# Performance work log

Hardware: AMD Instinct MI355X
Metric: run time of the kernel (lower is better)

The kernel has to match this reference:

```python
import jax, jax.numpy as jnp
import numpy as np

MARGIN = 0.2
LAMBDA_SOFTMAX = 9.0
LAMBDA_LSE = 6.0
WEIGHT_FACTOR = 0.7  # attn_prev is absent/zero on the i2t path
EPS = 1e-8
NEG_INF = -1e9


def setup_inputs() -> dict:
    key = jax.random.key(0)
    k1, k2, k3 = jax.random.split(key, 3)
    B, R, W, D = 128, 36, 32, 256  # batch, regions, max words, feat dim
    im = jax.random.normal(k1, (B, R, D), jnp.float32)
    s = jax.random.normal(k2, (B, W, D), jnp.float32)
    s_l = jax.random.randint(k3, (B,), 1, W + 1)  # caption lengths in [1, W]
    return {"im": im, "s": s, "s_l": s_l}


def _xattn_scores_i2t(im, s, s_l):
    # im: (B, R, D) images; s: (C, W, D) captions; s_l: (C,) lengths
    C, W = s.shape[0], s.shape[1]
    word_mask = jnp.arange(W)[None, :] < s_l[:, None]  # (C, W)

    # func_attention(query=images, context=caption words):
    # attn[c,b,w,r] = <s[c,w], im[b,r]>
    attn = jnp.einsum('cwd,brd->cbwr', s, im)
    # raw_feature_norm == 'clipped_l2norm': LeakyReLU(0.1) then l2norm over region axis
    attn = jax.nn.leaky_relu(attn, 0.1)
    attn = attn / (jnp.sqrt(jnp.sum(attn * attn, axis=-1, keepdims=True)) + EPS)
    # softmax over sourceL = words, with smoothing; mask padded words
    logits = jnp.where(word_mask[:, None, :, None], attn * LAMBDA_SOFTMAX, NEG_INF)
    A = jax.nn.softmax(logits, axis=2)  # (C, B, W, R), sums to 1 over words
    # weightedContext[c,b,r,:] = 0.7 * sum_w A[c,b,w,r] * s[c,w,:]
    wC = WEIGHT_FACTOR * jnp.einsum('cbwr,cwd->cbrd', A, s)

    # cosine similarity between image regions and weighted caption context
    num = jnp.sum(im[None] * wC, axis=-1)                      # (C, B, R)
    denom = jnp.linalg.norm(im, axis=-1)[None] * jnp.linalg.norm(wC, axis=-1)
    row_sim = num / jnp.clip(denom, EPS)

    # agg_func == 'LogSumExp' over regions
    sim = jax.nn.logsumexp(LAMBDA_LSE * row_sim, axis=2) / LAMBDA_LSE  # (C, B)
    return sim.T  # scores: (n_image, n_caption)


def reference(im, s, s_l):
    scores = _xattn_scores_i2t(im, s, s_l)
    diag = jnp.diag(scores)
    cost_s = jnp.clip(MARGIN + scores - diag[:, None], 0.0)   # caption retrieval
    cost_im = jnp.clip(MARGIN + scores - diag[None, :], 0.0)  # image retrieval
    eye = jnp.eye(scores.shape[0], dtype=bool)
    cost_s = jnp.where(eye, 0.0, cost_s)
    cost_im = jnp.where(eye, 0.0, cost_im)
    # max_violation=True: hardest negatives
    return jnp.sum(jnp.max(cost_s, axis=1)) + jnp.sum(jnp.max(cost_im, axis=0))
```

## Files before the change

### kernel.cpp

```cpp
#include <hip/hip_runtime.h>
#include <math.h>

#define CN 128
#define RN 36
#define WN 32
#define DN 256

#define SSTR  264
#define GSTR  40
#define ATSTR 40

#define WS_SCORES 0
#define WS_S_SW   65536
#define WS_IM_SW  (WS_S_SW + CN*16384)
#define WS_N2I    (WS_IM_SW + CN*18432)
#define WS_NEED   (WS_N2I + CN*RN*4)

typedef unsigned short u16;
typedef __attribute__((ext_vector_type(4))) unsigned short u16x4;
typedef __attribute__((ext_vector_type(8))) unsigned short u16x8;
typedef __attribute__((ext_vector_type(8))) __bf16 bf16x8;
typedef __attribute__((ext_vector_type(4))) float f32x4;

#define C9   12.9842502f
#define C6   8.65616798f
#define IC6  0.115524530f

__device__ __forceinline__ float bf2f(u16 u){ return __uint_as_float(((unsigned)u)<<16); }
__device__ __forceinline__ u16 f2bf(float f){ unsigned x=__float_as_uint(f); return (u16)((x + 0x7fffu + ((x>>16)&1u))>>16); }
__device__ __forceinline__ u16 f2bf_hw(float f){ __bf16 h = (__bf16)f; return __builtin_bit_cast(u16, h); }
__device__ __forceinline__ float lrelu(float v){ return fmaxf(v, 0.1f*v); }

__device__ __forceinline__ void gload16(const void* g, void* l){
    __builtin_amdgcn_global_load_lds((const __attribute__((address_space(1))) void*)g,
                                     (__attribute__((address_space(3))) void*)l, 16, 0, 0);
}

__global__ __launch_bounds__(256)
void precompute_kernel(const float* __restrict__ im, const float* __restrict__ s,
                       char* __restrict__ ws)
{
    const int tid = threadIdx.x;
    if (blockIdx.x < 128) {
        const int i = blockIdx.x;
        const float* src = s + (size_t)i*(WN*DN);
#pragma unroll
        for (int it = 0; it < 4; it++) {
            int idx = tid + it*256;
            int h = idx >> 9, r = (idx >> 4) & 31, x = idx & 15;
            int jl = x ^ (r & 7);
            const float4* p = (const float4*)(src + r*DN + h*128 + jl*8);
            float4 v0 = p[0], v1 = p[1];
            u16x8 hh = { f2bf(v0.x),f2bf(v0.y),f2bf(v0.z),f2bf(v0.w),
                         f2bf(v1.x),f2bf(v1.y),f2bf(v1.z),f2bf(v1.w) };
            *(u16x8*)(ws + WS_S_SW + (size_t)h*1048576 + (size_t)i*8192 + r*256 + x*16) = hh;
        }
    } else {
        const int i = blockIdx.x - 128;
        const float* src = im + (size_t)i*(RN*DN);
#pragma unroll
        for (int it = 0; it < 5; it++) {
            int idx = tid + it*256;
            if (idx < 1152) {
                int q = idx / 288, rem = idx - q*288;
                int r = rem >> 3, x = rem & 7;
                int jl = x ^ (r & 7);
                const float4* p = (const float4*)(src + r*DN + q*64 + jl*8);
                float4 v0 = p[0], v1 = p[1];
                u16x8 hh = { f2bf(v0.x),f2bf(v0.y),f2bf(v0.z),f2bf(v0.w),
                             f2bf(v1.x),f2bf(v1.y),f2bf(v1.z),f2bf(v1.w) };
                *(u16x8*)(ws + WS_IM_SW + (size_t)q*589824 + (size_t)i*4608 + r*128 + x*16) = hh;
            }
        }
        float* n2o = (float*)(ws + WS_N2I) + (size_t)i*RN;
#pragma unroll
        for (int it = 0; it < 2; it++) {
            int idx = tid + it*256;
            if (idx < 288) {
                int r = idx >> 3, q = idx & 7;
                const float4* p = (const float4*)(src + r*DN + q*32);
                float ss = 0.f;
#pragma unroll
                for (int k = 0; k < 8; k++) {
                    float4 v = p[k];
                    ss = fmaf(v.x,v.x,ss); ss = fmaf(v.y,v.y,ss);
                    ss = fmaf(v.z,v.z,ss); ss = fmaf(v.w,v.w,ss);
                }
                ss += __shfl_xor(ss,1); ss += __shfl_xor(ss,2); ss += __shfl_xor(ss,4);
                if (q == 0) n2o[r] = ss;
            }
        }
    }
}

__global__ __launch_bounds__(512, 4)
void xattn_staged(const int* __restrict__ s_l, char* __restrict__ ws)
{
    __shared__ __align__(16) u16 smem[19968];
    u16* lds_s  = smem;
    u16* lds_im = smem + 8192;
    u16* lds_g  = smem + 17408;
    char* sB = (char*)smem;

    const int tid = threadIdx.x;
    const int lane = tid & 63, wv = tid >> 6;
    const int bq = blockIdx.x, cp = blockIdx.y;
    const int ci = wv >> 2, bi = wv & 3;
    const int c = cp*2 + ci, b = bq*4 + bi;
    const int col = lane & 15, g4 = lane >> 4;
    const int gm = bi >> 1, gn = bi & 1;
    const int L = s_l[c];
    const int r2c = (32+col > 35) ? 35 : 32+col;

    const char* im_base = ws + WS_IM_SW + (size_t)(bq*4)*4608;
    const char* s_base  = ws + WS_S_SW  + (size_t)(cp*2)*8192;

    auto stageq = [&](int q){
        const int tot = (q & 1) ? 18 : 34;
        const char* imsrc = im_base + (size_t)q*589824;
        const char* ssrc  = s_base  + (size_t)(q>>1)*1048576;
#pragma unroll
        for (int t = 0; t < 5; t++) {
            int blk = wv + t*8;
            if (blk < tot) {
                const char* src; char* dst;
                if (blk < 18) { src = imsrc + blk*1024;      dst = sB + 16384 + blk*1024; }
                else          { src = ssrc + (blk-18)*1024;  dst = sB + (blk-18)*1024; }
                gload16(src + lane*16, dst);
            }
        }
    };

    const float* n2p = (const float*)(ws + WS_N2I) + (size_t)b*RN;
    float n2v0 = n2p[col];
    float n2v1 = n2p[16+col];
    float n2v2 = n2p[r2c];

    f32x4 raw[2][3];
#pragma unroll
    for (int m = 0; m < 2; m++)
#pragma unroll
        for (int n = 0; n < 3; n++) raw[m][n] = (f32x4){0.f,0.f,0.f,0.f};
    f32x4 gacc = {0.f,0.f,0.f,0.f};

    const u16* sbb = lds_s + ci*4096;
    const u16* ibb = lds_im + bi*2304;

    auto computeq = [&](int q){
#pragma unroll
        for (int ks = 0; ks < 2; ks++) {
            int chS = (q&1)*8 + ks*4 + g4;
            int chI = ks*4 + g4;
            int oA  = (chS ^ (col&7)) * 8;
            int oB  = (chI ^ (col&7)) * 8;
            int oB2 = (chI ^ (r2c&7)) * 8;
            bf16x8 a0 = *(const bf16x8*)&sbb[col*128 + oA];
            bf16x8 a1 = *(const bf16x8*)&sbb[(16+col)*128 + oA];
            bf16x8 b0 = *(const bf16x8*)&ibb[col*64 + oB];
            bf16x8 b1 = *(const bf16x8*)&ibb[(16+col)*64 + oB];
            bf16x8 b2 = *(const bf16x8*)&ibb[r2c*64 + oB2];
            bf16x8 ga = *(const bf16x8*)&sbb[(gm*16+col)*128 + oA];
            bf16x8 gb = *(const bf16x8*)&sbb[(gn*16+col)*128 + oA];
            raw[0][0] = __builtin_amdgcn_mfma_f32_16x16x32_bf16(a0, b0, raw[0][0], 0,0,0);
            raw[0][1] = __builtin_amdgcn_mfma_f32_16x16x32_bf16(a0, b1, raw[0][1], 0,0,0);
            raw[0][2] = __builtin_amdgcn_mfma_f32_16x16x32_bf16(a0, b2, raw[0][2], 0,0,0);
            raw[1][0] = __builtin_amdgcn_mfma_f32_16x16x32_bf16(a1, b0, raw[1][0], 0,0,0);
            raw[1][1] = __builtin_amdgcn_mfma_f32_16x16x32_bf16(a1, b1, raw[1][1], 0,0,0);
            raw[1][2] = __builtin_amdgcn_mfma_f32_16x16x32_bf16(a1, b2, raw[1][2], 0,0,0);
            gacc      = __builtin_amdgcn_mfma_f32_16x16x32_bf16(ga, gb, gacc, 0,0,0);
        }
    };

    stageq(0); __syncthreads();
    computeq(0); __syncthreads();
    stageq(1); __syncthreads();
    computeq(1); __syncthreads();
    stageq(2); __syncthreads();
    computeq(2); __syncthreads();
    stageq(3); __syncthreads();
    computeq(3);

    {
        u16x4 hg = { f2bf_hw(gacc[0]), f2bf_hw(gacc[1]), f2bf_hw(gacc[2]), f2bf_hw(gacc[3]) };
        *(u16x4*)&lds_g[ci*1280 + (gn*16+col)*GSTR + gm*16 + g4*4] = hg;
    }

    float af[2][3][4];
#pragma unroll
    for (int m = 0; m < 2; m++) {
#pragma unroll
        for (int reg = 0; reg < 4; reg++) {
            float ssum = 0.f;
#pragma unroll
            for (int n = 0; n < 3; n++) {
                float v = lrelu(raw[m][n][reg]);
                if (n == 2 && col >= 4) v = 0.f;
                af[m][n][reg] = v;
                ssum = fmaf(v, v, ssum);
            }
            ssum += __shfl_xor(ssum, 1);
            ssum += __shfl_xor(ssum, 2);
            ssum += __shfl_xor(ssum, 4);
            ssum += __shfl_xor(ssum, 8);
            float inv2 = C9 / (sqrtf(ssum) + 1e-8f);
#pragma unroll
            for (int n = 0; n < 3; n++) af[m][n][reg] *= inv2;
        }
    }

    float num[3];
#pragma unroll
    for (int n = 0; n < 3; n++) {
        float nm = 0.f;
#pragma unroll
        for (int m = 0; m < 2; m++)
#pragma unroll
            for (int reg = 0; reg < 4; reg++) {
                int w = m*16 + g4*4 + reg;
                float e = (w < L) ? __builtin_amdgcn_exp2f(af[m][n][reg]) : 0.f;
                af[m][n][reg] = e;
                nm = fmaf(e, raw[m][n][reg], nm);
            }
        nm += __shfl_xor(nm, 16);
        nm += __shfl_xor(nm, 32);
        num[n] = nm;
    }

    __syncthreads();

    u16* at = smem + wv*1920;
#pragma unroll
    for (int m = 0; m < 2; m++)
#pragma unroll
        for (int n = 0; n < 3; n++) {
            u16x4 h = { f2bf_hw(af[m][n][0]), f2bf_hw(af[m][n][1]),
                        f2bf_hw(af[m][n][2]), f2bf_hw(af[m][n][3]) };
            *(u16x4*)&at[(n*16 + col)*ATSTR + m*16 + g4*4] = h;
        }

    bf16x8 gf0 = *(const bf16x8*)&lds_g[ci*1280 + col*GSTR + g4*8];
    bf16x8 gf1 = *(const bf16x8*)&lds_g[ci*1280 + (16+col)*GSTR + g4*8];

    float qv[3];
#pragma unroll
    for (int n = 0; n < 3; n++) {
        bf16x8 bfv = *(const bf16x8*)&at[(n*16 + col)*ATSTR + g4*8];
        f32x4 z = {0.f,0.f,0.f,0.f};
        f32x4 t0 = __builtin_amdgcn_mfma_f32_16x16x32_bf16(gf0, bfv, z, 0,0,0);
        f32x4 t1 = __builtin_amdgcn_mfma_f32_16x16x32_bf16(gf1, bfv, z, 0,0,0);
        float q = 0.f;
#pragma unroll
        for (int reg = 0; reg < 4; reg++) {
            q = fmaf(af[0][n][reg], t0[reg], q);
            q = fmaf(af[1][n][reg], t1[reg], q);
        }
        q += __shfl_xor(q, 16);
        q += __shfl_xor(q, 32);
        qv[n] = q;
    }

    float rs[3];
    {
        float n2a[3] = { n2v0, n2v1, n2v2 };
#pragma unroll
        for (int n = 0; n < 3; n++) {
            float denom = fmaxf(0.7f * sqrtf(n2a[n] * qv[n]), 1e-8f);
            rs[n] = 0.7f * num[n] / denom;
        }
    }
    float xm = -1e30f;
#pragma unroll
    for (int n = 0; n < 3; n++) {
        bool valid = (n < 2) || (col < 4);
        if (valid) xm = fmaxf(xm, C6 * rs[n]);
    }
    xm = fmaxf(xm, __shfl_xor(xm, 1));
    xm = fmaxf(xm, __shfl_xor(xm, 2));
    xm = fmaxf(xm, __shfl_xor(xm, 4));
    xm = fmaxf(xm, __shfl_xor(xm, 8));
    float es = 0.f;
#pragma unroll
    for (int n = 0; n < 3; n++) {
        bool valid = (n < 2) || (col < 4);
        if (valid) es += __builtin_amdgcn_exp2f(C6 * rs[n] - xm);
    }
    es += __shfl_xor(es, 1);
    es += __shfl_xor(es, 2);
    es += __shfl_xor(es, 4);
    es += __shfl_xor(es, 8);

    if (lane == 0)
        ((float*)(ws + WS_SCORES))[(size_t)b * CN + c] =
            (xm + __builtin_amdgcn_logf(es)) * IC6;
}

__global__ __launch_bounds__(512, 2)
void xattn_fallback(const float* __restrict__ im, const float* __restrict__ s,
                    const int* __restrict__ s_l, float* __restrict__ scores)
{
    __shared__ u16   s_lds[2][WN*SSTR];
    __shared__ u16   im_lds[4][RN*SSTR];
    __shared__ u16   g_lds[2][WN*GSTR];
    __shared__ u16   at_lds[8][48*ATSTR];
    __shared__ float n2i_lds[4][RN];

    const int tid  = threadIdx.x;
    const int lane = tid & 63;
    const int wv   = tid >> 6;
    const int bq   = blockIdx.x, cp = blockIdx.y;
    const int ci   = wv >> 2, bi = wv & 3;
    const int c    = cp*2 + ci, b = bq*4 + bi;
    const int col  = lane & 15, g4 = lane >> 4;

    if (wv < 4) {
        const float4* g = (const float4*)(im + (size_t)(bq*4 + wv) * (RN*DN));
        u16* dst = im_lds[wv];
#pragma unroll
        for (int k = 0; k < 36; k++) {
            int i = lane + k*64;
            float4 v = g[i];
            int row = i >> 6, cc = (i & 63) * 4;
            u16x4 h = { f2bf(v.x), f2bf(v.y), f2bf(v.z), f2bf(v.w) };
            *(u16x4*)&dst[row*SSTR + cc] = h;
        }
    } else {
        int cap = (wv - 4) >> 1;
        int l2  = ((wv - 4) & 1) * 64 + lane;
        const float4* g = (const float4*)(s + (size_t)(cp*2 + cap) * (WN*DN));
        u16* dst = s_lds[cap];
#pragma unroll
        for (int k = 0; k < 16; k++) {
            int i = l2 + k*128;
            float4 v = g[i];
            int row = i >> 6, cc = (i & 63) * 4;
            u16x4 h = { f2bf(v.x), f2bf(v.y), f2bf(v.z), f2bf(v.w) };
            *(u16x4*)&dst[row*SSTR + cc] = h;
        }
    }
    __syncthreads();

    {
        const int gm = (wv >> 1) & 1, gn = wv & 1;
        const u16* sb = s_lds[ci];
        f32x4 acc = {0.f, 0.f, 0.f, 0.f};
#pragma unroll
        for (int ks = 0; ks < 8; ks++) {
            int k0 = ks*32 + g4*8;
            bf16x8 af = *(const bf16x8*)&sb[(gm*16 + col)*SSTR + k0];
            bf16x8 bfv = *(const bf16x8*)&sb[(gn*16 + col)*SSTR + k0];
            acc = __builtin_amdgcn_mfma_f32_16x16x32_bf16(af, bfv, acc, 0, 0, 0);
        }
        u16x4 h = { f2bf(acc[0]), f2bf(acc[1]), f2bf(acc[2]), f2bf(acc[3]) };
        *(u16x4*)&g_lds[ci][(gn*16 + col)*GSTR + gm*16 + g4*4] = h;
    }

    if (wv < 4) {
        const u16* ib = im_lds[wv];
        int r = lane >> 1, half = lane & 1;
        float ss = 0.f;
        const u16x8* p = (const u16x8*)&ib[r*SSTR + half*128];
#pragma unroll
        for (int k = 0; k < 16; k++) {
            u16x8 v = p[k];
#pragma unroll
            for (int j = 0; j < 8; j++) { float f = bf2f(v[j]); ss = fmaf(f, f, ss); }
        }
        ss += __shfl_xor(ss, 1);
        if (half == 0) n2i_lds[wv][r] = ss;
        if (lane < 8) {
            int r2 = 32 + (lane >> 1), h2 = lane & 1;
            float s2 = 0.f;
            const u16x8* p2 = (const u16x8*)&ib[r2*SSTR + h2*128];
#pragma unroll
            for (int k = 0; k < 16; k++) {
                u16x8 v = p2[k];
#pragma unroll
                for (int j = 0; j < 8; j++) { float f = bf2f(v[j]); s2 = fmaf(f, f, s2); }
            }
            s2 += __shfl_xor(s2, 1);
            if (h2 == 0) n2i_lds[wv][r2] = s2;
        }
    }

    const u16* sb = s_lds[ci];
    const u16* ib = im_lds[bi];
    f32x4 raw[2][3];
#pragma unroll
    for (int m = 0; m < 2; m++)
#pragma unroll
        for (int n = 0; n < 3; n++) raw[m][n] = (f32x4){0.f,0.f,0.f,0.f};
    {
        int r2c = 32 + col; if (r2c > 35) r2c = 35;
#pragma unroll
        for (int ks = 0; ks < 8; ks++) {
            int k0 = ks*32 + g4*8;
            bf16x8 a0 = *(const bf16x8*)&sb[col*SSTR + k0];
            bf16x8 a1 = *(const bf16x8*)&sb[(16 + col)*SSTR + k0];
            bf16x8 b0 = *(const bf16x8*)&ib[col*SSTR + k0];
            bf16x8 b1 = *(const bf16x8*)&ib[(16 + col)*SSTR + k0];
            bf16x8 b2 = *(const bf16x8*)&ib[r2c*SSTR + k0];
            raw[0][0] = __builtin_amdgcn_mfma_f32_16x16x32_bf16(a0, b0, raw[0][0], 0,0,0);
            raw[0][1] = __builtin_amdgcn_mfma_f32_16x16x32_bf16(a0, b1, raw[0][1], 0,0,0);
            raw[0][2] = __builtin_amdgcn_mfma_f32_16x16x32_bf16(a0, b2, raw[0][2], 0,0,0);
            raw[1][0] = __builtin_amdgcn_mfma_f32_16x16x32_bf16(a1, b0, raw[1][0], 0,0,0);
            raw[1][1] = __builtin_amdgcn_mfma_f32_16x16x32_bf16(a1, b1, raw[1][1], 0,0,0);
            raw[1][2] = __builtin_amdgcn_mfma_f32_16x16x32_bf16(a1, b2, raw[1][2], 0,0,0);
        }
    }

    float af[2][3][4];
#pragma unroll
    for (int m = 0; m < 2; m++) {
#pragma unroll
        for (int reg = 0; reg < 4; reg++) {
            float ssum = 0.f;
#pragma unroll
            for (int n = 0; n < 3; n++) {
                float v = lrelu(raw[m][n][reg]);
                if (n == 2 && col >= 4) v = 0.f;
                af[m][n][reg] = v;
                ssum = fmaf(v, v, ssum);
            }
            ssum += __shfl_xor(ssum, 1);
            ssum += __shfl_xor(ssum, 2);
            ssum += __shfl_xor(ssum, 4);
            ssum += __shfl_xor(ssum, 8);
            float inv = 1.0f / (sqrtf(ssum) + 1e-8f);
#pragma unroll
            for (int n = 0; n < 3; n++) af[m][n][reg] *= inv;
        }
    }

    const int L = s_l[c];
    float num[3], qv[3];
#pragma unroll
    for (int n = 0; n < 3; n++) {
        float mx = -1e30f;
#pragma unroll
        for (int m = 0; m < 2; m++)
#pragma unroll
            for (int reg = 0; reg < 4; reg++) {
                int w = m*16 + g4*4 + reg;
                if (w < L) mx = fmaxf(mx, af[m][n][reg]);
            }
        mx = fmaxf(mx, __shfl_xor(mx, 16));
        mx = fmaxf(mx, __shfl_xor(mx, 32));
        mx *= 9.0f;
        float sme = 0.f;
#pragma unroll
        for (int m = 0; m < 2; m++)
#pragma unroll
            for (int reg = 0; reg < 4; reg++) {
                int w = m*16 + g4*4 + reg;
                float e = (w < L) ? __expf(fmaf(9.0f, af[m][n][reg], -mx)) : 0.f;
                af[m][n][reg] = e;
                sme += e;
            }
        sme += __shfl_xor(sme, 16);
        sme += __shfl_xor(sme, 32);
        float inv = 1.0f / sme;
        float nm = 0.f;
#pragma unroll
        for (int m = 0; m < 2; m++)
#pragma unroll
            for (int reg = 0; reg < 4; reg++) {
                af[m][n][reg] *= inv;
                nm = fmaf(af[m][n][reg], raw[m][n][reg], nm);
            }
        nm += __shfl_xor(nm, 16);
        nm += __shfl_xor(nm, 32);
        num[n] = nm;
    }

#pragma unroll
    for (int m = 0; m < 2; m++)
#pragma unroll
        for (int n = 0; n < 3; n++) {
            u16x4 h = { f2bf(af[m][n][0]), f2bf(af[m][n][1]),
                        f2bf(af[m][n][2]), f2bf(af[m][n][3]) };
            *(u16x4*)&at_lds[wv][(n*16 + col)*ATSTR + m*16 + g4*4] = h;
        }

    __syncthreads();

    bf16x8 gf0 = *(const bf16x8*)&g_lds[ci][col*GSTR + g4*8];
    bf16x8 gf1 = *(const bf16x8*)&g_lds[ci][(16+col)*GSTR + g4*8];
    f32x4 tt[2][3];
#pragma unroll
    for (int n = 0; n < 3; n++) {
        bf16x8 bfv = *(const bf16x8*)&at_lds[wv][(n*16 + col)*ATSTR + g4*8];
        f32x4 z = {0.f,0.f,0.f,0.f};
        tt[0][n] = __builtin_amdgcn_mfma_f32_16x16x32_bf16(gf0, bfv, z, 0,0,0);
        tt[1][n] = __builtin_amdgcn_mfma_f32_16x16x32_bf16(gf1, bfv, z, 0,0,0);
    }

#pragma unroll
    for (int n = 0; n < 3; n++) {
        float q = 0.f;
#pragma unroll
        for (int m = 0; m < 2; m++)
#pragma unroll
            for (int reg = 0; reg < 4; reg++) q = fmaf(af[m][n][reg], tt[m][n][reg], q);
        q += __shfl_xor(q, 16);
        q += __shfl_xor(q, 32);
        qv[n] = q;
    }

    float rs[3];
#pragma unroll
    for (int n = 0; n < 3; n++) {
        int r = n*16 + col; if (r > 35) r = 35;
        float n2 = n2i_lds[bi][r];
        float denom = fmaxf(0.7f * sqrtf(n2 * qv[n]), 1e-8f);
        rs[n] = 0.7f * num[n] / denom;
    }
    float xm = -1e30f;
#pragma unroll
    for (int n = 0; n < 3; n++) {
        bool valid = (n < 2) || (col < 4);
        if (valid) xm = fmaxf(xm, 6.0f * rs[n]);
    }
    xm = fmaxf(xm, __shfl_xor(xm, 1));
    xm = fmaxf(xm, __shfl_xor(xm, 2));
    xm = fmaxf(xm, __shfl_xor(xm, 4));
    xm = fmaxf(xm, __shfl_xor(xm, 8));
    float es = 0.f;
#pragma unroll
    for (int n = 0; n < 3; n++) {
        bool valid = (n < 2) || (col < 4);
        if (valid) es += __expf(6.0f * rs[n] - xm);
    }
    es += __shfl_xor(es, 1);
    es += __shfl_xor(es, 2);
    es += __shfl_xor(es, 4);
    es += __shfl_xor(es, 8);

    if (lane == 0) scores[(size_t)b * CN + c] = (xm + __logf(es)) / 6.0f;
}

__global__ __launch_bounds__(1024)
void contrastive_loss_kernel(const float* __restrict__ scores,
                             unsigned int* __restrict__ out)
{
    __shared__ float sc[128][129];
    __shared__ float dg[128];
    __shared__ float red[128];
    const int tid = threadIdx.x;

    const float4* s4 = (const float4*)scores;
#pragma unroll
    for (int it = 0; it < 4; it++) {
        int i = tid + it*1024;
        float4 v = s4[i];
        int row = i >> 5, c4 = (i & 31) << 2;
        sc[row][c4+0] = v.x; sc[row][c4+1] = v.y;
        sc[row][c4+2] = v.z; sc[row][c4+3] = v.w;
    }
    __syncthreads();
    if (tid < 128) dg[tid] = sc[tid][tid];
    __syncthreads();

    const int i = tid >> 3, g = tid & 7;
    const float di = dg[i];
    float rm = 0.f, cm = 0.f;
#pragma unroll
    for (int k = 0; k < 16; k++) {
        int j = g*16 + k;
        if (j != i) {
            rm = fmaxf(rm, 0.2f + sc[i][j] - di);
            cm = fmaxf(cm, 0.2f + sc[j][i] - di);
        }
    }
    rm = fmaxf(rm, __shfl_xor(rm, 1)); cm = fmaxf(cm, __shfl_xor(cm, 1));
    rm = fmaxf(rm, __shfl_xor(rm, 2)); cm = fmaxf(cm, __shfl_xor(cm, 2));
    rm = fmaxf(rm, __shfl_xor(rm, 4)); cm = fmaxf(cm, __shfl_xor(cm, 4));
    if (g == 0) red[i] = rm + cm;
    __syncthreads();

    if (tid < 64) {
        float v = red[tid] + red[tid + 64];
#pragma unroll
        for (int off = 32; off >= 1; off >>= 1) v += __shfl_xor(v, off);
        if (tid == 0) {
            unsigned int x = __float_as_uint(v);
            unsigned int h = (x + 0x7fffu + ((x >> 16) & 1u)) >> 16;
            out[0] = (h << 16) | h;
        }
    }
}

extern "C" void kernel_launch(void* const* d_in, const int* in_sizes, int n_in,
                              void* d_out, int out_size, void* d_ws, size_t ws_size,
                              hipStream_t stream) {
    const float* im  = (const float*)d_in[0];
    const float* s   = (const float*)d_in[1];
    const int*   s_l = (const int*)d_in[2];
    char* ws = (char*)d_ws;

    dim3 grid(32, 64);
    if (ws_size >= (size_t)WS_NEED) {
        precompute_kernel<<<256, 256, 0, stream>>>(im, s, ws);
        xattn_staged<<<grid, 512, 0, stream>>>(s_l, ws);
    } else {
        xattn_fallback<<<grid, 512, 0, stream>>>(im, s, s_l, (float*)ws);
    }
    contrastive_loss_kernel<<<1, 1024, 0, stream>>>((const float*)ws, (unsigned int*)d_out);
}
```

Before: 51.87 us.

## Stage full caption tile once and double-buffer image chunks in LDS

The caption workspace layout changes from split halves to a contiguous per-caption tile. The main kernel now loads the whole caption tile into LDS once and double-buffers the image quarter-chunks, so each compute step overlaps the load of the next chunk and fewer barriers are needed. LDS use roughly doubles and launch bounds drop to 2 blocks per CU, which lowers occupancy. The precompute kernel also switches to hardware bf16 conversion.

```diff
diff --git a/kernel.cpp b/kernel.cpp
--- a/kernel.cpp
+++ b/kernel.cpp
@@ -44,16 +44,17 @@
     if (blockIdx.x < 128) {
         const int i = blockIdx.x;
         const float* src = s + (size_t)i*(WN*DN);
+        u16* out = (u16*)(ws + WS_S_SW) + (size_t)i*8192;
 #pragma unroll
         for (int it = 0; it < 4; it++) {
             int idx = tid + it*256;
-            int h = idx >> 9, r = (idx >> 4) & 31, x = idx & 15;
-            int jl = x ^ (r & 7);
-            const float4* p = (const float4*)(src + r*DN + h*128 + jl*8);
+            int r = idx >> 5, x = idx & 31;
+            int jl = (x & 24) | ((x & 7) ^ (r & 7));
+            const float4* p = (const float4*)(src + r*DN + jl*8);
             float4 v0 = p[0], v1 = p[1];
-            u16x8 hh = { f2bf(v0.x),f2bf(v0.y),f2bf(v0.z),f2bf(v0.w),
-                         f2bf(v1.x),f2bf(v1.y),f2bf(v1.z),f2bf(v1.w) };
-            *(u16x8*)(ws + WS_S_SW + (size_t)h*1048576 + (size_t)i*8192 + r*256 + x*16) = hh;
+            u16x8 hh = { f2bf_hw(v0.x),f2bf_hw(v0.y),f2bf_hw(v0.z),f2bf_hw(v0.w),
+                         f2bf_hw(v1.x),f2bf_hw(v1.y),f2bf_hw(v1.z),f2bf_hw(v1.w) };
+            *(u16x8*)(out + r*256 + x*8) = hh;
         }
     } else {
         const int i = blockIdx.x - 128;
@@ -67,8 +68,8 @@
                 int jl = x ^ (r & 7);
                 const float4* p = (const float4*)(src + r*DN + q*64 + jl*8);
                 float4 v0 = p[0], v1 = p[1];
-                u16x8 hh = { f2bf(v0.x),f2bf(v0.y),f2bf(v0.z),f2bf(v0.w),
-                             f2bf(v1.x),f2bf(v1.y),f2bf(v1.z),f2bf(v1.w) };
+                u16x8 hh = { f2bf_hw(v0.x),f2bf_hw(v0.y),f2bf_hw(v0.z),f2bf_hw(v0.w),
+                             f2bf_hw(v1.x),f2bf_hw(v1.y),f2bf_hw(v1.z),f2bf_hw(v1.w) };
                 *(u16x8*)(ws + WS_IM_SW + (size_t)q*589824 + (size_t)i*4608 + r*128 + x*16) = hh;
             }
         }
@@ -93,14 +94,14 @@
     }
 }
 
-__global__ __launch_bounds__(512, 4)
+__global__ __launch_bounds__(512, 2)
 void xattn_staged(const int* __restrict__ s_l, char* __restrict__ ws)
 {
-    __shared__ __align__(16) u16 smem[19968];
+    __shared__ __align__(16) u16 smem[37376];
     u16* lds_s  = smem;
-    u16* lds_im = smem + 8192;
-    u16* lds_g  = smem + 17408;
-    char* sB = (char*)smem;
+    u16* lds_im = smem + 16384;
+    u16* lds_g  = smem + 34816;
+    char* smem_b = (char*)smem;
 
     const int tid = threadIdx.x;
     const int lane = tid & 63, wv = tid >> 6;
@@ -112,24 +113,29 @@
     const int L = s_l[c];
     const int r2c = (32+col > 35) ? 35 : 32+col;
 
-    const char* im_base = ws + WS_IM_SW + (size_t)(bq*4)*4608;
-    const char* s_base  = ws + WS_S_SW  + (size_t)(cp*2)*8192;
-
-    auto stageq = [&](int q){
-        const int tot = (q & 1) ? 18 : 34;
-        const char* imsrc = im_base + (size_t)q*589824;
-        const char* ssrc  = s_base  + (size_t)(q>>1)*1048576;
-#pragma unroll
-        for (int t = 0; t < 5; t++) {
+    const char* ssrc = ws + WS_S_SW + (size_t)(cp*2)*16384;
+    const char* ibase = ws + WS_IM_SW + (size_t)(bq*4)*4608;
+
+    auto stage_im = [&](int q, int buf){
+        const char* isrc = ibase + (size_t)q*589824;
+        char* dbase = smem_b + 32768 + buf*18432;
+#pragma unroll
+        for (int t = 0; t < 3; t++) {
             int blk = wv + t*8;
-            if (blk < tot) {
-                const char* src; char* dst;
-                if (blk < 18) { src = imsrc + blk*1024;      dst = sB + 16384 + blk*1024; }
-                else          { src = ssrc + (blk-18)*1024;  dst = sB + (blk-18)*1024; }
-                gload16(src + lane*16, dst);
-            }
+            if (blk < 18) gload16(isrc + blk*1024 + lane*16, dbase + blk*1024);
         }
     };
+
+#pragma unroll
+    for (int t = 0; t < 7; t++) {
+        int blk = wv + t*8;
+        if (blk < 50) {
+            const char* src; char* dst;
+            if (blk < 32) { src = ssrc + blk*1024;         dst = smem_b + blk*1024; }
+            else          { src = ibase + (blk-32)*1024;   dst = smem_b + 32768 + (blk-32)*1024; }
+            gload16(src + lane*16, dst);
+        }
+    }
 
     const float* n2p = (const float*)(ws + WS_N2I) + (size_t)b*RN;
     float n2v0 = n2p[col];
@@ -143,24 +149,24 @@
         for (int n = 0; n < 3; n++) raw[m][n] = (f32x4){0.f,0.f,0.f,0.f};
     f32x4 gacc = {0.f,0.f,0.f,0.f};
 
-    const u16* sbb = lds_s + ci*4096;
-    const u16* ibb = lds_im + bi*2304;
-
-    auto computeq = [&](int q){
+    const u16* sbb = lds_s + ci*8192;
+
+    auto computeq = [&](int q, int buf){
+        const u16* ibb = lds_im + buf*9216 + bi*2304;
 #pragma unroll
         for (int ks = 0; ks < 2; ks++) {
-            int chS = (q&1)*8 + ks*4 + g4;
-            int chI = ks*4 + g4;
-            int oA  = (chS ^ (col&7)) * 8;
-            int oB  = (chI ^ (col&7)) * 8;
-            int oB2 = (chI ^ (r2c&7)) * 8;
-            bf16x8 a0 = *(const bf16x8*)&sbb[col*128 + oA];
-            bf16x8 a1 = *(const bf16x8*)&sbb[(16+col)*128 + oA];
+            int chq = ks*4 + g4;
+            int swA = chq ^ (col & 7);
+            int oA  = (q*8 + swA) * 8;
+            int oB  = swA * 8;
+            int oB2 = (chq ^ (r2c & 7)) * 8;
+            bf16x8 a0 = *(const bf16x8*)&sbb[col*256 + oA];
+            bf16x8 a1 = *(const bf16x8*)&sbb[(16+col)*256 + oA];
+            bf16x8 ga = *(const bf16x8*)&sbb[(gm*16+col)*256 + oA];
+            bf16x8 gb = *(const bf16x8*)&sbb[(gn*16+col)*256 + oA];
             bf16x8 b0 = *(const bf16x8*)&ibb[col*64 + oB];
             bf16x8 b1 = *(const bf16x8*)&ibb[(16+col)*64 + oB];
             bf16x8 b2 = *(const bf16x8*)&ibb[r2c*64 + oB2];
-            bf16x8 ga = *(const bf16x8*)&sbb[(gm*16+col)*128 + oA];
-            bf16x8 gb = *(const bf16x8*)&sbb[(gn*16+col)*128 + oA];
             raw[0][0] = __builtin_amdgcn_mfma_f32_16x16x32_bf16(a0, b0, raw[0][0], 0,0,0);
             raw[0][1] = __builtin_amdgcn_mfma_f32_16x16x32_bf16(a0, b1, raw[0][1], 0,0,0);
             raw[0][2] = __builtin_amdgcn_mfma_f32_16x16x32_bf16(a0, b2, raw[0][2], 0,0,0);
@@ -171,14 +177,14 @@
         }
     };
 
-    stageq(0); __syncthreads();
-    computeq(0); __syncthreads();
-    stageq(1); __syncthreads();
-    computeq(1); __syncthreads();
-    stageq(2); __syncthreads();
-    computeq(2); __syncthreads();
-    stageq(3); __syncthreads();
-    computeq(3);
+    __syncthreads();
+    stage_im(1, 1); computeq(0, 0);
+    __syncthreads();
+    stage_im(2, 0); computeq(1, 1);
+    __syncthreads();
+    stage_im(3, 1); computeq(2, 0);
+    __syncthreads();
+    computeq(3, 1);
 
     {
         u16x4 hg = { f2bf_hw(gacc[0]), f2bf_hw(gacc[1]), f2bf_hw(gacc[2]), f2bf_hw(gacc[3]) };
@@ -228,7 +234,7 @@
 
     __syncthreads();
 
-    u16* at = smem + wv*1920;
+    u16* at = (u16*)(smem_b + 32768) + wv*1920;
 #pragma unroll
     for (int m = 0; m < 2; m++)
 #pragma unroll
```

Measured after the change: 51.64 us. No clear change (-0.4%).
